# Kernel optimization log

Hardware: AMD Instinct MI355X
Metric: run time of the kernel (lower is better)

Reference implementation:

```python
import jax, jax.numpy as jnp
import numpy as np

B, S, D, H = 2, 2048, 1024, 16
HD = D // H

def setup_inputs() -> dict:
    key = jax.random.key(0)
    ks = jax.random.split(key, 9)
    s = 1.0 / np.sqrt(D)
    return {
        "x": jax.random.normal(ks[0], (B, S, D), jnp.float32),
        "Wq": jax.random.normal(ks[1], (D, D), jnp.float32) * s,
        "bq": jnp.zeros((D,), jnp.float32),
        "Wk": jax.random.normal(ks[2], (D, D), jnp.float32) * s,
        "bk": jnp.zeros((D,), jnp.float32),
        "Wv": jax.random.normal(ks[3], (D, D), jnp.float32) * s,
        "bv": jnp.zeros((D,), jnp.float32),
        "Wo": jax.random.normal(ks[4], (D, D), jnp.float32) * s,
        "bo": jnp.zeros((D,), jnp.float32),
    }

def reference(x, Wq, bq, Wk, bk, Wv, bv, Wo, bo):
    b, s, d = x.shape
    def split_heads(t):
        return t.reshape(b, s, H, HD).transpose(0, 2, 1, 3)  # [B,H,S,HD]
    q = split_heads(x @ Wq + bq)
    k = split_heads(x @ Wk + bk)
    v = split_heads(x @ Wv + bv)
    scores = jnp.einsum('bhqd,bhkd->bhqk', q, k) / jnp.sqrt(jnp.float32(HD))
    causal = jnp.tril(jnp.ones((s, s), bool))  # True = keep
    scores = jnp.where(causal, scores, -jnp.inf)
    attn = jax.nn.softmax(scores, axis=-1)
    out = jnp.einsum('bhqk,bhkd->bhqd', attn, v)  # [B,H,S,HD]
    out = out.transpose(0, 2, 1, 3).reshape(b, s, d)
    return out @ Wo + bo
```

## Files before the change

### kernel.cpp

```cpp
#include <hip/hip_runtime.h>

typedef unsigned short u16;
typedef unsigned int u32;
typedef __attribute__((ext_vector_type(8))) short bf16x8;
typedef __attribute__((ext_vector_type(4))) float f32x4;

#define BB 2
#define SS 2048
#define DD 1024
#define HH 16
#define HD 64
#define MM (BB * SS)

__device__ inline float u2f(u32 u) { return __uint_as_float(u); }
__device__ inline u16 f2bf(float f) {
  u32 u = __float_as_uint(f);
  return (u16)((u + 0x7fffu + ((u >> 16) & 1u)) >> 16);
}

__device__ inline int sw(int r, int ci) { return r * 64 + (((ci ^ (r & 7)) & 7) << 3); }

typedef const __attribute__((address_space(1))) void* gas_ptr;
typedef __attribute__((address_space(3))) void* las_ptr;
__device__ __forceinline__ void gll16(const void* g, void* l) {
  __builtin_amdgcn_global_load_lds((gas_ptr)g, (las_ptr)l, 16, 0, 0);
}

__device__ __forceinline__ u32 pk2(float a, float b) {
  return (__float_as_uint(a) >> 16) | (__float_as_uint(b) & 0xffff0000u);
}

__global__ __launch_bounds__(256) void prep(const float* __restrict__ x, u16* __restrict__ xb,
                                            const float* __restrict__ W0, const float* __restrict__ W1,
                                            const float* __restrict__ W2, const float* __restrict__ W3,
                                            u16* __restrict__ Wt) {
  int z = blockIdx.z;
  int t = threadIdx.x;
  if (z >= 4) {
    int gid = (z - 4) * 256 + blockIdx.y * 16 + blockIdx.x;
    int i = (gid * 256 + t) * 8;
    float4 a = *(const float4*)(x + i);
    float4 b = *(const float4*)(x + i + 4);
    uint4 o;
    o.x = (u32)f2bf(a.x) | ((u32)f2bf(a.y) << 16);
    o.y = (u32)f2bf(a.z) | ((u32)f2bf(a.w) << 16);
    o.z = (u32)f2bf(b.x) | ((u32)f2bf(b.y) << 16);
    o.w = (u32)f2bf(b.z) | ((u32)f2bf(b.w) << 16);
    *(uint4*)(xb + i) = o;
    return;
  }
  const float* W = (z == 0) ? W0 : (z == 1) ? W1 : (z == 2) ? W2 : W3;
  u16* out = Wt + (size_t)z * (DD * DD);
  __shared__ __align__(16) u16 T[64][72];
  int n0 = blockIdx.x * 64, k0 = blockIdx.y * 64;
#pragma unroll
  for (int p = 0; p < 4; ++p) {
    int kr = (t >> 4) + p * 16;
    int c4 = (t & 15) * 4;
    float4 v = *(const float4*)&W[(size_t)(k0 + kr) * DD + n0 + c4];
    T[c4 + 0][kr] = f2bf(v.x);
    T[c4 + 1][kr] = f2bf(v.y);
    T[c4 + 2][kr] = f2bf(v.z);
    T[c4 + 3][kr] = f2bf(v.w);
  }
  __syncthreads();
#pragma unroll
  for (int p = 0; p < 2; ++p) {
    int n = (t >> 3) + p * 32;
    int c8 = (t & 7) * 8;
    uint4 v = *(const uint4*)&T[n][c8];
    *(uint4*)&out[(size_t)(n0 + n) * DD + k0 + c8] = v;
  }
}

__global__ __launch_bounds__(256, 3) void gemm_qkv(const u16* __restrict__ xb, const u16* __restrict__ Wt,
                                                   const float* __restrict__ bq, const float* __restrict__ bk,
                                                   const float* __restrict__ bv,
                                                   u16* __restrict__ Qb, u16* __restrict__ Kb, u16* __restrict__ Vtb) {
  __shared__ __align__(16) u16 As[2][128 * 32];
  __shared__ __align__(16) u16 Bs[2][128 * 32];
  const int tid = threadIdx.x, lane = tid & 63, wv = tid >> 6;
  const int wm = (wv >> 1) * 64, wn = (wv & 1) * 64;
  const int l16 = lane & 15, quad = lane >> 4;

  const int id = blockIdx.x;
  const int xcd = id & 7, inner = id >> 3;
  const int mg = xcd >> 1, ng = xcd & 1;
  const int im = inner & 7, rest = inner >> 3;
  const int in_ = rest & 3, z = rest >> 2;
  const int m0 = (mg * 8 + im) * 128, n0 = (ng * 4 + in_) * 128;

  const u16* Bt = Wt + (size_t)z * (DD * DD);
  const float* bias = (z == 0) ? bq : (z == 1) ? bk : bv;

  const int r0 = tid >> 2, k8 = (tid & 3) << 3;
  const u16* Ap0 = &xb[(size_t)(m0 + r0) * DD + k8];
  const u16* Ap1 = Ap0 + (size_t)64 * DD;
  const u16* Bp0 = &Bt[(size_t)(n0 + r0) * DD + k8];
  const u16* Bp1 = Bp0 + (size_t)64 * DD;

  gll16(Ap0, &As[0][wv * 512]);
  gll16(Ap1, &As[0][2048 + wv * 512]);
  gll16(Bp0, &Bs[0][wv * 512]);
  gll16(Bp1, &Bs[0][2048 + wv * 512]);

  f32x4 acc[4][4];
  f32x4 zero = {0.f, 0.f, 0.f, 0.f};
#pragma unroll
  for (int i = 0; i < 4; ++i)
#pragma unroll
    for (int j = 0; j < 4; ++j) acc[i][j] = zero;

  __syncthreads();

  for (int kk = 0; kk < 32; ++kk) {
    const int cur = kk & 1;
    if (kk + 1 < 32) {
      const int nxt = cur ^ 1;
      const int ko = (kk + 1) * 32;
      gll16(Ap0 + ko, &As[nxt][wv * 512]);
      gll16(Ap1 + ko, &As[nxt][2048 + wv * 512]);
      gll16(Bp0 + ko, &Bs[nxt][wv * 512]);
      gll16(Bp1 + ko, &Bs[nxt][2048 + wv * 512]);
    }
    bf16x8 af[4], bg[4];
#pragma unroll
    for (int i = 0; i < 4; ++i) {
      af[i] = *(const bf16x8*)&As[cur][(wm + i * 16 + l16) * 32 + quad * 8];
      bg[i] = *(const bf16x8*)&Bs[cur][(wn + i * 16 + l16) * 32 + quad * 8];
    }
#pragma unroll
    for (int i = 0; i < 4; ++i)
#pragma unroll
      for (int j = 0; j < 4; ++j)
        acc[i][j] = __builtin_amdgcn_mfma_f32_16x16x32_bf16(af[i], bg[j], acc[i][j], 0, 0, 0);
    __syncthreads();
  }

  const float qsc = (z == 0) ? 0.180336880f : 1.0f;
  if (z == 2) {
#pragma unroll
    for (int i = 0; i < 4; ++i) {
#pragma unroll
      for (int j = 0; j < 4; ++j) {
        int col = n0 + wn + j * 16 + l16;
        float bcol = bias[col];
        int hh = col >> 6, dd = col & 63;
        int row0 = m0 + wm + i * 16;
        int bb = row0 >> 11, s0 = row0 & (SS - 1);
        int sbase = (s0 & ~63) + (i >> 1) * 32 + quad * 8 + (i & 1) * 4;
        size_t base = (((size_t)((bb * HH + hh) * HD + dd)) << 11) + sbase;
        uint2 pv;
        pv.x = (u32)f2bf(acc[i][j][0] + bcol) | ((u32)f2bf(acc[i][j][1] + bcol) << 16);
        pv.y = (u32)f2bf(acc[i][j][2] + bcol) | ((u32)f2bf(acc[i][j][3] + bcol) << 16);
        *(uint2*)&Vtb[base] = pv;
      }
    }
  } else {
    u16* out = (z == 0) ? Qb : Kb;
#pragma unroll
    for (int i = 0; i < 4; ++i) {
#pragma unroll
      for (int j = 0; j < 4; ++j) {
        int col = n0 + wn + j * 16 + l16;
        float bcol = bias[col];
        int hh = col >> 6, dd = col & 63;
#pragma unroll
        for (int r = 0; r < 4; ++r) {
          int row = m0 + wm + i * 16 + quad * 4 + r;
          int bb = row >> 11, s = row & (SS - 1);
          out[((size_t)((bb * HH + hh) * SS + s) << 6) | dd] = f2bf((acc[i][j][r] + bcol) * qsc);
        }
      }
    }
  }
}

__global__ __launch_bounds__(256, 3) void gemm_out(const u16* __restrict__ Ub, const u16* __restrict__ Wot,
                                                   const float* __restrict__ bo, float* __restrict__ out) {
  __shared__ __align__(16) u16 As[2][128 * 32];
  __shared__ __align__(16) u16 Bs[2][64 * 32];
  const int tid = threadIdx.x, lane = tid & 63, wv = tid >> 6;
  const int wm = (wv >> 1) * 64, wn = (wv & 1) * 32;
  const int l16 = lane & 15, quad = lane >> 4;
  const int r0 = tid >> 2, k8 = (tid & 3) << 3;

  const int id = blockIdx.x;
  const int xcd = id & 7, inner = id >> 3;
  const int mg = xcd >> 1, ng = xcd & 1;
  const int im = inner & 7, in_ = inner >> 3;
  const int m0 = (mg * 8 + im) * 128, n0 = (ng * 8 + in_) * 64;

  const u16* Ap0 = &Ub[(size_t)(m0 + r0) * DD + k8];
  const u16* Ap1 = Ap0 + (size_t)64 * DD;
  const u16* Bp0 = &Wot[(size_t)(n0 + r0) * DD + k8];

  gll16(Ap0, &As[0][wv * 512]);
  gll16(Ap1, &As[0][2048 + wv * 512]);
  gll16(Bp0, &Bs[0][wv * 512]);

  f32x4 acc[4][2];
  f32x4 zero = {0.f, 0.f, 0.f, 0.f};
#pragma unroll
  for (int i = 0; i < 4; ++i) { acc[i][0] = zero; acc[i][1] = zero; }

  __syncthreads();

  for (int kk = 0; kk < 32; ++kk) {
    const int cur = kk & 1;
    if (kk + 1 < 32) {
      const int nxt = cur ^ 1;
      const int ko = (kk + 1) * 32;
      gll16(Ap0 + ko, &As[nxt][wv * 512]);
      gll16(Ap1 + ko, &As[nxt][2048 + wv * 512]);
      gll16(Bp0 + ko, &Bs[nxt][wv * 512]);
    }
    bf16x8 af[4], bg[2];
#pragma unroll
    for (int i = 0; i < 4; ++i) af[i] = *(const bf16x8*)&As[cur][(wm + i * 16 + l16) * 32 + quad * 8];
#pragma unroll
    for (int j = 0; j < 2; ++j) bg[j] = *(const bf16x8*)&Bs[cur][(wn + j * 16 + l16) * 32 + quad * 8];
#pragma unroll
    for (int i = 0; i < 4; ++i)
#pragma unroll
      for (int j = 0; j < 2; ++j)
        acc[i][j] = __builtin_amdgcn_mfma_f32_16x16x32_bf16(af[i], bg[j], acc[i][j], 0, 0, 0);
    __syncthreads();
  }

#pragma unroll
  for (int i = 0; i < 4; ++i) {
#pragma unroll
    for (int j = 0; j < 2; ++j) {
      int col = n0 + wn + j * 16 + l16;
      float bcol = bo[col];
#pragma unroll
      for (int r = 0; r < 4; ++r) {
        int row = m0 + wm + i * 16 + quad * 4 + r;
        out[(size_t)row * DD + col] = acc[i][j][r] + bcol;
      }
    }
  }
}

__global__ __launch_bounds__(256, 4) void attention_mfma(const u16* __restrict__ Q, const u16* __restrict__ K,
                                                         const u16* __restrict__ Vt, u16* __restrict__ Uo) {
  const int tid = threadIdx.x, lane = tid & 63, wv = tid >> 6;
  const int l16 = lane & 15, quad = lane >> 4;
  const int bh = blockIdx.x & 31;
  const int b = bh >> 4, h = bh & 15;
  const int qt = 31 - (blockIdx.x >> 5);
  const int q0 = qt * 64;
  const u16* Qh = Q + (size_t)(b * HH + h) * SS * HD;
  const u16* Kh = K + (size_t)(b * HH + h) * SS * HD;
  const u16* Vh = Vt + (size_t)(b * HH + h) * HD * SS;

  __shared__ __align__(16) u16 K_lds[2][64 * 64];
  __shared__ __align__(16) u16 V_lds[2][64 * 64];

  bf16x8 qf0, qf1;
  {
    const u16* qp = &Qh[(size_t)(q0 + wv * 16 + l16) * HD + quad * 8];
    qf0 = *(const bf16x8*)qp;
    qf1 = *(const bf16x8*)(qp + 32);
  }

  f32x4 zero = {0.f, 0.f, 0.f, 0.f};
  f32x4 o[4];
#pragma unroll
  for (int j = 0; j < 4; ++j) o[j] = zero;
  float lsum = 0.f;

  const int sr = tid >> 2, ci = tid & 3, cc = ci << 3;
  const u16* Kg = &Kh[(size_t)sr * HD + cc];
  const u16* Vg = &Vh[(size_t)sr * SS + cc];
  const int ktiles = qt + 1;
  const int wlo = sw(sr, ci), whi = sw(sr, ci + 4);

  uint4 ka = *(const uint4*)Kg, kb = *(const uint4*)(Kg + 32);
  uint4 va = *(const uint4*)Vg, vb = *(const uint4*)(Vg + 32);
  *(uint4*)&K_lds[0][wlo] = ka;
  *(uint4*)&K_lds[0][whi] = kb;
  *(uint4*)&V_lds[0][wlo] = va;
  *(uint4*)&V_lds[0][whi] = vb;
  {
    const u16* Kn = Kg + (size_t)64 * HD;
    const u16* Vn = Vg + 64;
    ka = *(const uint4*)Kn; kb = *(const uint4*)(Kn + 32);
    va = *(const uint4*)Vn; vb = *(const uint4*)(Vn + 32);
  }
  __syncthreads();

  for (int t = 0; t < ktiles; ++t) {
    const int cur = t & 1;

    f32x4 sT[4];
#pragma unroll
    for (int n = 0; n < 4; ++n) {
      const int kr = n * 16 + l16;
      bf16x8 kf0 = *(const bf16x8*)&K_lds[cur][sw(kr, quad)];
      bf16x8 kf1 = *(const bf16x8*)&K_lds[cur][sw(kr, quad + 4)];
      f32x4 a = zero;
      a = __builtin_amdgcn_mfma_f32_16x16x32_bf16(kf0, qf0, a, 0, 0, 0);
      a = __builtin_amdgcn_mfma_f32_16x16x32_bf16(kf1, qf1, a, 0, 0, 0);
      sT[n] = a;
    }

    float p[4][4];
#pragma unroll
    for (int n = 0; n < 4; ++n)
#pragma unroll
      for (int r = 0; r < 4; ++r) p[n][r] = __builtin_amdgcn_exp2f(sT[n][r]);
    if (t == qt) {
      const int qloc = wv * 16 + l16;
#pragma unroll
      for (int n = 0; n < 4; ++n)
#pragma unroll
        for (int r = 0; r < 4; ++r)
          if (n * 16 + quad * 4 + r > qloc) p[n][r] = 0.f;
    }
#pragma unroll
    for (int n = 0; n < 4; ++n) lsum += (p[n][0] + p[n][1]) + (p[n][2] + p[n][3]);

    union { uint4 u; bf16x8 v; } pa0, pa1;
    pa0.u.x = pk2(p[0][0], p[0][1]);
    pa0.u.y = pk2(p[0][2], p[0][3]);
    pa0.u.z = pk2(p[1][0], p[1][1]);
    pa0.u.w = pk2(p[1][2], p[1][3]);
    pa1.u.x = pk2(p[2][0], p[2][1]);
    pa1.u.y = pk2(p[2][2], p[2][3]);
    pa1.u.z = pk2(p[3][0], p[3][1]);
    pa1.u.w = pk2(p[3][2], p[3][3]);

#pragma unroll
    for (int j = 0; j < 4; ++j) {
      const int vr = j * 16 + l16;
      bf16x8 vf0 = *(const bf16x8*)&V_lds[cur][sw(vr, quad)];
      bf16x8 vf1 = *(const bf16x8*)&V_lds[cur][sw(vr, quad + 4)];
      o[j] = __builtin_amdgcn_mfma_f32_16x16x32_bf16(pa0.v, vf0, o[j], 0, 0, 0);
      o[j] = __builtin_amdgcn_mfma_f32_16x16x32_bf16(pa1.v, vf1, o[j], 0, 0, 0);
    }

    if (t + 1 < ktiles) {
      const int nxt = cur ^ 1;
      *(uint4*)&K_lds[nxt][wlo] = ka;
      *(uint4*)&K_lds[nxt][whi] = kb;
      *(uint4*)&V_lds[nxt][wlo] = va;
      *(uint4*)&V_lds[nxt][whi] = vb;
      if (t + 2 < ktiles) {
        const u16* Kn = Kg + (size_t)(t + 2) * 64 * HD;
        const u16* Vn = Vg + (t + 2) * 64;
        ka = *(const uint4*)Kn; kb = *(const uint4*)(Kn + 32);
        va = *(const uint4*)Vn; vb = *(const uint4*)(Vn + 32);
      }
    }
    __syncthreads();
  }

  lsum += __shfl_xor(lsum, 16);
  lsum += __shfl_xor(lsum, 32);
  float linv[4];
#pragma unroll
  for (int r = 0; r < 4; ++r) linv[r] = 1.0f / __shfl(lsum, quad * 4 + r);

#pragma unroll
  for (int j = 0; j < 4; ++j) {
#pragma unroll
    for (int r = 0; r < 4; ++r) {
      int row = q0 + wv * 16 + quad * 4 + r;
      Uo[(size_t)(b * SS + row) * DD + (h << 6) + j * 16 + l16] = f2bf(o[j][r] * linv[r]);
    }
  }
}

extern "C" void kernel_launch(void* const* d_in, const int* in_sizes, int n_in,
                              void* d_out, int out_size, void* d_ws, size_t ws_size,
                              hipStream_t stream) {
  const float* x  = (const float*)d_in[0];
  const float* Wq = (const float*)d_in[1];
  const float* bq = (const float*)d_in[2];
  const float* Wk = (const float*)d_in[3];
  const float* bk = (const float*)d_in[4];
  const float* Wv = (const float*)d_in[5];
  const float* bv = (const float*)d_in[6];
  const float* Wo = (const float*)d_in[7];
  const float* bo = (const float*)d_in[8];
  float* out = (float*)d_out;

  char* ws = (char*)d_ws;
  u16* xb  = (u16*)(ws);
  u16* Wt  = (u16*)(ws + ((size_t)8 << 20));
  u16* Qb  = (u16*)(ws + ((size_t)16 << 20));
  u16* Kb  = (u16*)(ws + ((size_t)24 << 20));
  u16* Vtb = (u16*)(ws + ((size_t)32 << 20));
  u16* Ub  = (u16*)(ws + ((size_t)40 << 20));

  prep<<<dim3(16, 16, 12), dim3(256), 0, stream>>>(x, xb, Wq, Wk, Wv, Wo, Wt);
  gemm_qkv<<<dim3(768), dim3(256), 0, stream>>>(xb, Wt, bq, bk, bv, Qb, Kb, Vtb);
  attention_mfma<<<dim3(1024), dim3(256), 0, stream>>>(Qb, Kb, Vtb, Ub);
  gemm_out<<<dim3(512), dim3(256), 0, stream>>>(Ub, Wt + (size_t)3 * DD * DD, bo, out);
}
```

Before: 173.6 us.

## Switch attention to 32x32 MFMA with 128-row query blocks and padded LDS

Rewrites the attention kernel to use 32x32x16 bf16 MFMA tiles, with each wave owning 32 query rows and each block covering 128 rows. The grid is halved and paired so that long and short causal blocks are balanced across launches. The XOR-swizzled LDS layout is replaced by a padded one, and the V-transpose store order in the QKV GEMM is changed to match. This should cut K/V reloads per query and the number of MFMA instructions issued, at the cost of more registers (occupancy hint drops from 4 to 2) and a causal skip test per wave.

New measurement: 170.7 us. No clear change (-1.7%).

```diff
diff --git a/kernel.cpp b/kernel.cpp
--- a/kernel.cpp
+++ b/kernel.cpp
@@ -4,6 +4,7 @@
 typedef unsigned int u32;
 typedef __attribute__((ext_vector_type(8))) short bf16x8;
 typedef __attribute__((ext_vector_type(4))) float f32x4;
+typedef __attribute__((ext_vector_type(16))) float f32x16;
 
 #define BB 2
 #define SS 2048
@@ -17,8 +18,6 @@
   u32 u = __float_as_uint(f);
   return (u16)((u + 0x7fffu + ((u >> 16) & 1u)) >> 16);
 }
-
-__device__ inline int sw(int r, int ci) { return r * 64 + (((ci ^ (r & 7)) & 7) << 3); }
 
 typedef const __attribute__((address_space(1))) void* gas_ptr;
 typedef __attribute__((address_space(3))) void* las_ptr;
@@ -148,7 +147,7 @@
         int hh = col >> 6, dd = col & 63;
         int row0 = m0 + wm + i * 16;
         int bb = row0 >> 11, s0 = row0 & (SS - 1);
-        int sbase = (s0 & ~63) + (i >> 1) * 32 + quad * 8 + (i & 1) * 4;
+        int sbase = (s0 & ~63) + i * 16 + ((quad & 1) << 3) + ((quad >> 1) << 2);
         size_t base = (((size_t)((bb * HH + hh) * HD + dd)) << 11) + sbase;
         uint2 pv;
         pv.x = (u32)f2bf(acc[i][j][0] + bcol) | ((u32)f2bf(acc[i][j][1] + bcol) << 16);
@@ -243,46 +242,48 @@
   }
 }
 
-__global__ __launch_bounds__(256, 4) void attention_mfma(const u16* __restrict__ Q, const u16* __restrict__ K,
+__global__ __launch_bounds__(256, 2) void attention_mfma(const u16* __restrict__ Q, const u16* __restrict__ K,
                                                          const u16* __restrict__ Vt, u16* __restrict__ Uo) {
   const int tid = threadIdx.x, lane = tid & 63, wv = tid >> 6;
-  const int l16 = lane & 15, quad = lane >> 4;
+  const int l31 = lane & 31, hi = lane >> 5;
   const int bh = blockIdx.x & 31;
   const int b = bh >> 4, h = bh & 15;
-  const int qt = 31 - (blockIdx.x >> 5);
-  const int q0 = qt * 64;
+  const int g = blockIdx.x >> 5;
+  const int qb = (blockIdx.x < 256) ? (15 - g) : (g - 8);
+  const int q0 = qb * 128;
+  const int qbase = q0 + wv * 32;
   const u16* Qh = Q + (size_t)(b * HH + h) * SS * HD;
   const u16* Kh = K + (size_t)(b * HH + h) * SS * HD;
   const u16* Vh = Vt + (size_t)(b * HH + h) * HD * SS;
 
-  __shared__ __align__(16) u16 K_lds[2][64 * 64];
-  __shared__ __align__(16) u16 V_lds[2][64 * 64];
-
-  bf16x8 qf0, qf1;
+  __shared__ __align__(16) u16 K_lds[2][4160];
+  __shared__ __align__(16) u16 V_lds[2][4160];
+  __shared__ float lsc[128];
+
+  bf16x8 qf[4];
   {
-    const u16* qp = &Qh[(size_t)(q0 + wv * 16 + l16) * HD + quad * 8];
-    qf0 = *(const bf16x8*)qp;
-    qf1 = *(const bf16x8*)(qp + 32);
-  }
-
-  f32x4 zero = {0.f, 0.f, 0.f, 0.f};
-  f32x4 o[4];
-#pragma unroll
-  for (int j = 0; j < 4; ++j) o[j] = zero;
+    const u16* qp = &Qh[(size_t)(qbase + l31) * HD + 8 * hi];
+#pragma unroll
+    for (int m = 0; m < 4; ++m) qf[m] = *(const bf16x8*)(qp + 16 * m);
+  }
+
+  f32x16 o0, o1;
+#pragma unroll
+  for (int i = 0; i < 16; ++i) { o0[i] = 0.f; o1[i] = 0.f; }
   float lsum = 0.f;
 
-  const int sr = tid >> 2, ci = tid & 3, cc = ci << 3;
-  const u16* Kg = &Kh[(size_t)sr * HD + cc];
-  const u16* Vg = &Vh[(size_t)sr * SS + cc];
-  const int ktiles = qt + 1;
-  const int wlo = sw(sr, ci), whi = sw(sr, ci + 4);
+  const int sr = tid >> 2, ci = tid & 3;
+  const u16* Kg = &Kh[(size_t)sr * HD + ci * 8];
+  const u16* Vg = &Vh[(size_t)sr * SS + ci * 8];
+  const int ktiles = 2 * qb + 2;
+  const int w0 = ci * 520 + sr * 8, w1 = (ci + 4) * 520 + sr * 8;
 
   uint4 ka = *(const uint4*)Kg, kb = *(const uint4*)(Kg + 32);
   uint4 va = *(const uint4*)Vg, vb = *(const uint4*)(Vg + 32);
-  *(uint4*)&K_lds[0][wlo] = ka;
-  *(uint4*)&K_lds[0][whi] = kb;
-  *(uint4*)&V_lds[0][wlo] = va;
-  *(uint4*)&V_lds[0][whi] = vb;
+  *(uint4*)&K_lds[0][w0] = ka;
+  *(uint4*)&K_lds[0][w1] = kb;
+  *(uint4*)&V_lds[0][w0] = va;
+  *(uint4*)&V_lds[0][w1] = vb;
   {
     const u16* Kn = Kg + (size_t)64 * HD;
     const u16* Vn = Vg + 64;
@@ -293,60 +294,65 @@
 
   for (int t = 0; t < ktiles; ++t) {
     const int cur = t & 1;
-
-    f32x4 sT[4];
-#pragma unroll
-    for (int n = 0; n < 4; ++n) {
-      const int kr = n * 16 + l16;
-      bf16x8 kf0 = *(const bf16x8*)&K_lds[cur][sw(kr, quad)];
-      bf16x8 kf1 = *(const bf16x8*)&K_lds[cur][sw(kr, quad + 4)];
-      f32x4 a = zero;
-      a = __builtin_amdgcn_mfma_f32_16x16x32_bf16(kf0, qf0, a, 0, 0, 0);
-      a = __builtin_amdgcn_mfma_f32_16x16x32_bf16(kf1, qf1, a, 0, 0, 0);
-      sT[n] = a;
-    }
-
-    float p[4][4];
-#pragma unroll
-    for (int n = 0; n < 4; ++n)
-#pragma unroll
-      for (int r = 0; r < 4; ++r) p[n][r] = __builtin_amdgcn_exp2f(sT[n][r]);
-    if (t == qt) {
-      const int qloc = wv * 16 + l16;
-#pragma unroll
-      for (int n = 0; n < 4; ++n)
-#pragma unroll
-        for (int r = 0; r < 4; ++r)
-          if (n * 16 + quad * 4 + r > qloc) p[n][r] = 0.f;
-    }
-#pragma unroll
-    for (int n = 0; n < 4; ++n) lsum += (p[n][0] + p[n][1]) + (p[n][2] + p[n][3]);
-
-    union { uint4 u; bf16x8 v; } pa0, pa1;
-    pa0.u.x = pk2(p[0][0], p[0][1]);
-    pa0.u.y = pk2(p[0][2], p[0][3]);
-    pa0.u.z = pk2(p[1][0], p[1][1]);
-    pa0.u.w = pk2(p[1][2], p[1][3]);
-    pa1.u.x = pk2(p[2][0], p[2][1]);
-    pa1.u.y = pk2(p[2][2], p[2][3]);
-    pa1.u.z = pk2(p[3][0], p[3][1]);
-    pa1.u.w = pk2(p[3][2], p[3][3]);
-
-#pragma unroll
-    for (int j = 0; j < 4; ++j) {
-      const int vr = j * 16 + l16;
-      bf16x8 vf0 = *(const bf16x8*)&V_lds[cur][sw(vr, quad)];
-      bf16x8 vf1 = *(const bf16x8*)&V_lds[cur][sw(vr, quad + 4)];
-      o[j] = __builtin_amdgcn_mfma_f32_16x16x32_bf16(pa0.v, vf0, o[j], 0, 0, 0);
-      o[j] = __builtin_amdgcn_mfma_f32_16x16x32_bf16(pa1.v, vf1, o[j], 0, 0, 0);
+    if (64 * t <= qbase + 31) {
+      f32x16 s0, s1;
+#pragma unroll
+      for (int i = 0; i < 16; ++i) { s0[i] = 0.f; s1[i] = 0.f; }
+#pragma unroll
+      for (int m = 0; m < 4; ++m) {
+        const u16* kp = &K_lds[cur][(2 * m + hi) * 520 + l31 * 8];
+        bf16x8 kf0 = *(const bf16x8*)kp;
+        bf16x8 kf1 = *(const bf16x8*)(kp + 256);
+        s0 = __builtin_amdgcn_mfma_f32_32x32x16_bf16(kf0, qf[m], s0, 0, 0, 0);
+        s1 = __builtin_amdgcn_mfma_f32_32x32x16_bf16(kf1, qf[m], s1, 0, 0, 0);
+      }
+#pragma unroll
+      for (int i = 0; i < 16; ++i) {
+        s0[i] = __builtin_amdgcn_exp2f(s0[i]);
+        s1[i] = __builtin_amdgcn_exp2f(s1[i]);
+      }
+      if (64 * t + 63 > qbase) {
+        const int qq = qbase + l31, kb0 = 64 * t + 4 * hi;
+#pragma unroll
+        for (int p = 0; p < 4; ++p)
+#pragma unroll
+          for (int c = 0; c < 4; ++c) {
+            if (kb0 + 8 * p + c > qq) s0[4 * p + c] = 0.f;
+            if (kb0 + 32 + 8 * p + c > qq) s1[4 * p + c] = 0.f;
+          }
+      }
+#pragma unroll
+      for (int i = 0; i < 16; ++i) lsum += s0[i] + s1[i];
+
+#pragma unroll
+      for (int m = 0; m < 4; ++m) {
+        const int p0 = 8 * (m & 1);
+        union { uint4 u; bf16x8 v; } pa;
+        if (m < 2) {
+          pa.u.x = pk2(s0[p0 + 0], s0[p0 + 1]);
+          pa.u.y = pk2(s0[p0 + 2], s0[p0 + 3]);
+          pa.u.z = pk2(s0[p0 + 4], s0[p0 + 5]);
+          pa.u.w = pk2(s0[p0 + 6], s0[p0 + 7]);
+        } else {
+          pa.u.x = pk2(s1[p0 + 0], s1[p0 + 1]);
+          pa.u.y = pk2(s1[p0 + 2], s1[p0 + 3]);
+          pa.u.z = pk2(s1[p0 + 4], s1[p0 + 5]);
+          pa.u.w = pk2(s1[p0 + 6], s1[p0 + 7]);
+        }
+        const u16* vp = &V_lds[cur][(2 * m + hi) * 520 + l31 * 8];
+        bf16x8 vf0 = *(const bf16x8*)vp;
+        bf16x8 vf1 = *(const bf16x8*)(vp + 256);
+        o0 = __builtin_amdgcn_mfma_f32_32x32x16_bf16(pa.v, vf0, o0, 0, 0, 0);
+        o1 = __builtin_amdgcn_mfma_f32_32x32x16_bf16(pa.v, vf1, o1, 0, 0, 0);
+      }
     }
 
     if (t + 1 < ktiles) {
       const int nxt = cur ^ 1;
-      *(uint4*)&K_lds[nxt][wlo] = ka;
-      *(uint4*)&K_lds[nxt][whi] = kb;
-      *(uint4*)&V_lds[nxt][wlo] = va;
-      *(uint4*)&V_lds[nxt][whi] = vb;
+      *(uint4*)&K_lds[nxt][w0] = ka;
+      *(uint4*)&K_lds[nxt][w1] = kb;
+      *(uint4*)&V_lds[nxt][w0] = va;
+      *(uint4*)&V_lds[nxt][w1] = vb;
       if (t + 2 < ktiles) {
         const u16* Kn = Kg + (size_t)(t + 2) * 64 * HD;
         const u16* Vn = Vg + (t + 2) * 64;
@@ -357,18 +363,21 @@
     __syncthreads();
   }
 
-  lsum += __shfl_xor(lsum, 16);
   lsum += __shfl_xor(lsum, 32);
-  float linv[4];
-#pragma unroll
-  for (int r = 0; r < 4; ++r) linv[r] = 1.0f / __shfl(lsum, quad * 4 + r);
-
-#pragma unroll
-  for (int j = 0; j < 4; ++j) {
-#pragma unroll
-    for (int r = 0; r < 4; ++r) {
-      int row = q0 + wv * 16 + quad * 4 + r;
-      Uo[(size_t)(b * SS + row) * DD + (h << 6) + j * 16 + l16] = f2bf(o[j][r] * linv[r]);
+  if (hi == 0) lsc[wv * 32 + l31] = 1.0f / lsum;
+  __syncthreads();
+  f32x4 lv[4];
+#pragma unroll
+  for (int p = 0; p < 4; ++p) lv[p] = *(const f32x4*)&lsc[wv * 32 + 8 * p + 4 * hi];
+
+  u16* ub = Uo + (size_t)(b * SS) * DD + (h << 6);
+#pragma unroll
+  for (int p = 0; p < 4; ++p) {
+#pragma unroll
+    for (int c = 0; c < 4; ++c) {
+      int row = qbase + 8 * p + 4 * hi + c;
+      ub[(size_t)row * DD + l31] = f2bf(o0[4 * p + c] * lv[p][c]);
+      ub[(size_t)row * DD + 32 + l31] = f2bf(o1[4 * p + c] * lv[p][c]);
     }
   }
 }
@@ -397,6 +406,6 @@
 
   prep<<<dim3(16, 16, 12), dim3(256), 0, stream>>>(x, xb, Wq, Wk, Wv, Wo, Wt);
   gemm_qkv<<<dim3(768), dim3(256), 0, stream>>>(xb, Wt, bq, bk, bv, Qb, Kb, Vtb);
-  attention_mfma<<<dim3(1024), dim3(256), 0, stream>>>(Qb, Kb, Vtb, Ub);
+  attention_mfma<<<dim3(512), dim3(256), 0, stream>>>(Qb, Kb, Vtb, Ub);
   gemm_out<<<dim3(512), dim3(256), 0, stream>>>(Ub, Wt + (size_t)3 * DD * DD, bo, out);
 }
```
